# Performance work log

Measured on AMD Instinct MI355X. Metric: run time of the kernel, lower is better.

Reference implementation:

```python
import jax, jax.numpy as jnp
import numpy as np

N_U, N_P, E, E_LAB = 100000, 50000, 2000000, 500000
D_U, D_P, H = 64, 128, 64


def _seg_mean(feat, idx, n):
    # scatter-mean: sum per destination / clamp(count, 1)
    s = jax.ops.segment_sum(feat, idx, num_segments=n)
    c = jax.ops.segment_sum(jnp.ones((idx.shape[0],), feat.dtype), idx, num_segments=n)
    return s / jnp.maximum(c, 1.0)[:, None]


def setup_inputs() -> dict:
    key = jax.random.key(0)
    ks = jax.random.split(key, 16)
    inp = {
        'x_user': jax.random.normal(ks[0], (N_U, D_U), jnp.float32),
        'x_product': jax.random.normal(ks[1], (N_P, D_P), jnp.float32),
        'W1_buys_l': jax.random.normal(ks[2], (D_U, H), jnp.float32) * 0.05,
        'b1_buys': jnp.zeros((H,), jnp.float32),
        'W1_buys_r': jax.random.normal(ks[3], (D_P, H), jnp.float32) * 0.05,
        'W1_rev_l': jax.random.normal(ks[4], (D_P, H), jnp.float32) * 0.05,
        'b1_rev': jnp.zeros((H,), jnp.float32),
        'W1_rev_r': jax.random.normal(ks[5], (D_U, H), jnp.float32) * 0.05,
        'W2_buys_l': jax.random.normal(ks[6], (H, H), jnp.float32) * 0.05,
        'b2_buys': jnp.zeros((H,), jnp.float32),
        'W2_buys_r': jax.random.normal(ks[7], (H, H), jnp.float32) * 0.05,
        'W2_rev_l': jax.random.normal(ks[8], (H, H), jnp.float32) * 0.05,
        'b2_rev': jnp.zeros((H,), jnp.float32),
        'W2_rev_r': jax.random.normal(ks[9], (H, H), jnp.float32) * 0.05,
        'edge_src': jax.random.randint(ks[10], (E,), 0, N_U, jnp.int32),
        'edge_dst': jax.random.randint(ks[11], (E,), 0, N_P, jnp.int32),
        'lab_u': jax.random.randint(ks[12], (E_LAB,), 0, N_U, jnp.int32),
        'lab_p': jax.random.randint(ks[13], (E_LAB,), 0, N_P, jnp.int32),
    }
    return inp


def reference(x_user, x_product, W1_buys_l, b1_buys, W1_buys_r, W1_rev_l, b1_rev, W1_rev_r,
              W2_buys_l, b2_buys, W2_buys_r, W2_rev_l, b2_rev, W2_rev_r,
              edge_src, edge_dst, lab_u, lab_p):
    # SAGEConv (mean aggr): out_dst = mean_agg(x_src) @ W_l + b + x_dst @ W_r
    def sage(x_src, x_dst, src, dst, n_dst, Wl, b, Wr):
        agg = _seg_mean(x_src[src], dst, n_dst)
        return agg @ Wl + b + x_dst @ Wr

    n_u, n_p = x_user.shape[0], x_product.shape[0]
    # layer 1 (per edge type, hetero) + relu
    h_p = jax.nn.relu(sage(x_user, x_product, edge_src, edge_dst, n_p, W1_buys_l, b1_buys, W1_buys_r))
    h_u = jax.nn.relu(sage(x_product, x_user, edge_dst, edge_src, n_u, W1_rev_l, b1_rev, W1_rev_r))
    # layer 2
    h_p2 = sage(h_u, h_p, edge_src, edge_dst, n_p, W2_buys_l, b2_buys, W2_buys_r)
    h_u2 = sage(h_p, h_u, edge_dst, edge_src, n_u, W2_rev_l, b2_rev, W2_rev_r)
    # classifier: per-label-edge dot product
    return jnp.sum(h_u2[lab_u] * h_p2[lab_p], axis=-1)
```

## Files before the change

### kernel.cpp

```cpp
#include <hip/hip_runtime.h>


using u16 = unsigned short;
using u32 = unsigned int;

__device__ __forceinline__ u16 bf16r(float f) {
    u32 b = __float_as_uint(f);
    b += 0x7fffu + ((b >> 16) & 1u);
    return (u16)(b >> 16);
}
__device__ __forceinline__ float bflo(u32 u) { return __uint_as_float(u << 16); }
__device__ __forceinline__ float bfhi(u32 u) { return __uint_as_float(u & 0xffff0000u); }

#define BSH 8
#define MAXB 512
#define CHUNK 4096
#define RPT 16

__global__ __launch_bounds__(256) void k_partCast(
    const int* __restrict__ keysP, const int* __restrict__ payP,
    int* __restrict__ curPp, uint2* __restrict__ pairsP, int NBP, int SLP,
    const int* __restrict__ keysU, const int* __restrict__ payU,
    int* __restrict__ curUp, uint2* __restrict__ pairsU, int NBU, int SLU,
    int E, int pblocks,
    const int* __restrict__ keysL,
    int* __restrict__ curLp, uint2* __restrict__ pairsL, int NBL, int SLL,
    int EL, int lblocks,
    const float* __restrict__ xc, u16* __restrict__ yc, int n8) {
    __shared__ int hist[MAXB];
    __shared__ int sA[MAXB];
    __shared__ int sB[MAXB];
    __shared__ int bx[MAXB];
    __shared__ int gbase[MAXB];
    __shared__ uint2 prs[CHUNK];
    int tid = threadIdx.x;
    int bix = blockIdx.x;
    if (bix >= 2 * pblocks + lblocks) {
        int i = (bix - 2 * pblocks - lblocks) * 256 + tid;
        if (i < n8) {
            const float4* x4 = (const float4*)xc;
            float4 a = x4[i * 2], b = x4[i * 2 + 1];
            uint4 o;
            o.x = (u32)bf16r(a.x) | ((u32)bf16r(a.y) << 16);
            o.y = (u32)bf16r(a.z) | ((u32)bf16r(a.w) << 16);
            o.z = (u32)bf16r(b.x) | ((u32)bf16r(b.y) << 16);
            o.w = (u32)bf16r(b.z) | ((u32)bf16r(b.w) << 16);
            ((uint4*)yc)[i] = o;
        }
        return;
    }
    const int* keys; const int* pay; int* cursor; uint2* pairs;
    int NB, SL, cb, nE;
    if (bix < pblocks) {
        keys = keysP; pay = payP; cursor = curPp; pairs = pairsP; NB = NBP; SL = SLP;
        cb = bix; nE = E;
    } else if (bix < 2 * pblocks) {
        keys = keysU; pay = payU; cursor = curUp; pairs = pairsU; NB = NBU; SL = SLU;
        cb = bix - pblocks; nE = E;
    } else {
        keys = keysL; pay = nullptr; cursor = curLp; pairs = pairsL; NB = NBL; SL = SLL;
        cb = bix - 2 * pblocks; nE = EL;
    }
    int i0 = cb * CHUNK;
    int count = min(CHUNK, nE - i0);
    for (int i = tid; i < MAXB; i += 256) hist[i] = 0;
    __syncthreads();
    int keyr[RPT], payr[RPT], rankr[RPT];
#pragma unroll
    for (int r = 0; r < RPT; ++r) {
        int idx = r * 256 + tid;
        if (idx < count) {
            int k = keys[i0 + idx];
            keyr[r] = k;
            payr[r] = pay ? pay[i0 + idx] : (i0 + idx);
            rankr[r] = atomicAdd(&hist[k >> BSH], 1);
        } else keyr[r] = -1;
    }
    __syncthreads();
    sA[tid] = hist[tid]; sA[tid + 256] = hist[tid + 256];
    __syncthreads();
    int* src = sA; int* dst = sB;
    for (int off = 1; off < MAXB; off <<= 1) {
        dst[tid] = src[tid] + ((tid >= off) ? src[tid - off] : 0);
        int i2 = tid + 256;
        dst[i2] = src[i2] + ((i2 >= off) ? src[i2 - off] : 0);
        __syncthreads();
        int* t = src; src = dst; dst = t;
    }
    bx[tid] = src[tid] - hist[tid];
    bx[tid + 256] = src[tid + 256] - hist[tid + 256];
    __syncthreads();
    for (int b = tid; b < NB; b += 256) {
        int c = hist[b];
        gbase[b] = c ? (b * SL + atomicAdd(&cursor[b], c)) : 0;
    }
#pragma unroll
    for (int r = 0; r < RPT; ++r) {
        if (keyr[r] >= 0)
            prs[bx[keyr[r] >> BSH] + rankr[r]] = make_uint2((u32)keyr[r], (u32)payr[r]);
    }
    __syncthreads();
    for (int j = tid; j < count; j += 256) {
        uint2 pr = prs[j];
        int b = pr.x >> BSH;
        pairs[gbase[b] + (j - bx[b])] = pr;
    }
}

__global__ __launch_bounds__(256) void k_bucketFill(
    const uint2* __restrict__ pairsP, const int* __restrict__ cntP, int NBP, int SLP,
    int* __restrict__ nbr_p, int* __restrict__ deg_p, int* __restrict__ ptr_p, int NP,
    const uint2* __restrict__ pairsU, const int* __restrict__ cntU, int NBU, int SLU,
    int* __restrict__ nbr_u, int* __restrict__ deg_u, int* __restrict__ ptr_u, int NU) {
    const uint2* pairs; const int* cntA; int* nbr; int* deg; int* ptr;
    int N, SL, bucket;
    if ((int)blockIdx.x < NBP) {
        pairs = pairsP; cntA = cntP; nbr = nbr_p; deg = deg_p; ptr = ptr_p; N = NP;
        SL = SLP; bucket = blockIdx.x;
    } else {
        pairs = pairsU; cntA = cntU; nbr = nbr_u; deg = deg_u; ptr = ptr_u; N = NU;
        SL = SLU; bucket = blockIdx.x - NBP;
    }
    int tid = threadIdx.x;
    int base = bucket * SL;
    int cnt = cntA[bucket];
    __shared__ int h[256];
    __shared__ int s[256];
    __shared__ int cur[256];
    h[tid] = 0;
    __syncthreads();
    for (int j = tid; j < cnt; j += 256) atomicAdd(&h[pairs[base + j].x & 255], 1);
    __syncthreads();
    int d = h[tid];
    s[tid] = d;
    __syncthreads();
    for (int off = 1; off < 256; off <<= 1) {
        int v = (tid >= off) ? s[tid - off] : 0;
        __syncthreads();
        s[tid] += v;
        __syncthreads();
    }
    int excl = s[tid] - d;
    int node = bucket * 256 + tid;
    if (node < N) { deg[node] = d; ptr[node] = base + excl; }
    cur[tid] = excl;
    __syncthreads();
    for (int j = tid; j < cnt; j += 256) {
        uint2 pr = pairs[base + j];
        int pos = atomicAdd(&cur[pr.x & 255], 1);
        nbr[base + pos] = (int)(pr.y << 7);
    }
}

#define ACC8(A0,A1,A2,A3,A4,A5,A6,A7,V) \
    A0 += bflo((V).x); A1 += bfhi((V).x); A2 += bflo((V).y); A3 += bfhi((V).y); \
    A4 += bflo((V).z); A5 += bfhi((V).z); A6 += bflo((V).w); A7 += bfhi((V).w);

__global__ __launch_bounds__(256) void k_gather2(
    const u16* __restrict__ yA, const int* __restrict__ nbrA, const int* __restrict__ stpA,
    const int* __restrict__ degA, float* __restrict__ aggA, int NA,
    const u16* __restrict__ yB, const int* __restrict__ nbrB, const int* __restrict__ stpB,
    const int* __restrict__ degB, float* __restrict__ aggB, int NB) {
    int w = (blockIdx.x * 256 + threadIdx.x) >> 6;
    int lane = threadIdx.x & 63;
    if (w >= NA + NB) return;
    const u16* y; const int* nbr; const int* stp; const int* deg; float* agg; int n;
    if (w < NA) { y = yA; nbr = nbrA; stp = stpA; deg = degA; agg = aggA; n = w; }
    else        { y = yB; nbr = nbrB; stp = stpB; deg = degB; agg = aggB; n = w - NA; }
    const int q = lane >> 3, t = lane & 7;
    const int d = deg[n];
    const int st = stp[n];
    const char* yb = (const char*)y + t * 16;
    float a0=0,a1=0,a2=0,a3=0,a4=0,a5=0,a6=0,a7=0;
    for (int j = 0; j < d; j += 64) {
        const int cnt = min(d - j, 64);
        int offv = 0;
        if (lane < cnt) offv = nbr[st + j + lane];
#define GLD(R) \
        int g##R = __shfl(offv, R * 8 + q, 64); \
        uint4 v##R = make_uint4(0u, 0u, 0u, 0u); \
        if (R * 8 + q < cnt) v##R = *(const uint4*)(yb + g##R);
        GLD(0) GLD(1) GLD(2) GLD(3) GLD(4) GLD(5) GLD(6) GLD(7)
#undef GLD
#define ACCR(R) if (R * 8 < cnt) { ACC8(a0,a1,a2,a3,a4,a5,a6,a7,v##R) }
        ACCR(0) ACCR(1) ACCR(2) ACCR(3) ACCR(4) ACCR(5) ACCR(6) ACCR(7)
#undef ACCR
    }
#pragma unroll
    for (int m = 8; m < 64; m <<= 1) {
        a0 += __shfl_xor(a0, m, 64); a1 += __shfl_xor(a1, m, 64);
        a2 += __shfl_xor(a2, m, 64); a3 += __shfl_xor(a3, m, 64);
        a4 += __shfl_xor(a4, m, 64); a5 += __shfl_xor(a5, m, 64);
        a6 += __shfl_xor(a6, m, 64); a7 += __shfl_xor(a7, m, 64);
    }
    if (q == 0) {
        float dinv = 1.0f / (float)max(d, 1);
        float* dstp = agg + n * 64 + t * 8;
        *(float4*)dstp       = make_float4(a0 * dinv, a1 * dinv, a2 * dinv, a3 * dinv);
        *(float4*)(dstp + 4) = make_float4(a4 * dinv, a5 * dinv, a6 * dinv, a7 * dinv);
    }
}

#define FMA_ROW(ACC, O, W4) \
    ACC[0] += (O) * (W4).x; ACC[1] += (O) * (W4).y; \
    ACC[2] += (O) * (W4).z; ACC[3] += (O) * (W4).w;

template <int K, bool PRE, bool BIAS, bool RELU, bool EMIT>
__global__ __launch_bounds__(256) void k_ctilePairX(
    const float* __restrict__ pre0, const float* __restrict__ bias0,
    const float* __restrict__ x0, const float* __restrict__ W0,
    float* __restrict__ h0, u16* __restrict__ hbf0, int N0, int g0,
    const float* __restrict__ pre1, const float* __restrict__ bias1,
    const float* __restrict__ x1, const float* __restrict__ W1,
    float* __restrict__ h1, u16* __restrict__ hbf1, int N1) {
    constexpr int ROWS = (K == 64) ? 64 : 32;
    constexpr int RR = ROWS / 16;
    constexpr int STRIDE = K + 4;
    constexpr int KF4 = K / 4;
    __shared__ float Ws[K * 64];
    __shared__ float op[ROWS * STRIDE];
    const float* pre; const float* bias; const float* x; const float* W;
    float* h; u16* hbf;
    int N, bid, gsz;
    if ((int)blockIdx.x < g0) {
        pre = pre0; bias = bias0; x = x0; W = W0; h = h0; hbf = hbf0; N = N0;
        bid = blockIdx.x; gsz = g0;
    } else {
        pre = pre1; bias = bias1; x = x1; W = W1; h = h1; hbf = hbf1; N = N1;
        bid = blockIdx.x - g0; gsz = gridDim.x - g0;
    }
    const int tid = threadIdx.x;
    for (int i = tid; i < K * 16; i += 256)
        ((float4*)Ws)[i] = ((const float4*)W)[i];
    const int c4 = (tid & 15) * 4;
    const int rb = (tid >> 4) * RR;
    float bx_ = 0.f, by_ = 0.f, bz_ = 0.f, bw_ = 0.f;
    if (BIAS) {
        float4 b4 = *(const float4*)(bias + c4);
        bx_ = b4.x; by_ = b4.y; bz_ = b4.z; bw_ = b4.w;
    }
    const int ntiles = (N + ROWS - 1) / ROWS;
    for (int tile = bid; tile < ntiles; tile += gsz) {
        const int row0 = tile * ROWS;
        __syncthreads();
        for (int i = tid; i < ROWS * KF4; i += 256) {
            int r = i / KF4, k4 = (i % KF4) * 4;
            int row = row0 + r;
            float4 v = make_float4(0.f, 0.f, 0.f, 0.f);
            if (row < N) v = *(const float4*)(x + (size_t)row * K + k4);
            *(float4*)(op + r * STRIDE + k4) = v;
        }
        __syncthreads();
        float acc[RR][4];
#pragma unroll
        for (int i = 0; i < RR; ++i) {
            float px = 0.f, py = 0.f, pz = 0.f, pw = 0.f;
            if (PRE) {
                int row = row0 + rb + i;
                if (row < N) {
                    float4 p = *(const float4*)(pre + row * 64 + c4);
                    px = p.x; py = p.y; pz = p.z; pw = p.w;
                }
            }
            acc[i][0] = bx_ + px; acc[i][1] = by_ + py;
            acc[i][2] = bz_ + pz; acc[i][3] = bw_ + pw;
        }
        for (int kk = 0; kk < K; kk += 4) {
            float4 w0 = *(const float4*)(Ws + (kk + 0) * 64 + c4);
            float4 w1 = *(const float4*)(Ws + (kk + 1) * 64 + c4);
            float4 w2 = *(const float4*)(Ws + (kk + 2) * 64 + c4);
            float4 w3 = *(const float4*)(Ws + (kk + 3) * 64 + c4);
#pragma unroll
            for (int i = 0; i < RR; ++i) {
                float4 o = *(const float4*)(op + (rb + i) * STRIDE + kk);
                FMA_ROW(acc[i], o.x, w0);
                FMA_ROW(acc[i], o.y, w1);
                FMA_ROW(acc[i], o.z, w2);
                FMA_ROW(acc[i], o.w, w3);
            }
        }
#pragma unroll
        for (int i = 0; i < RR; ++i) {
            int row = row0 + rb + i;
            if (row >= N) continue;
            float v0 = acc[i][0], v1 = acc[i][1], v2 = acc[i][2], v3 = acc[i][3];
            if (RELU) {
                v0 = fmaxf(v0, 0.f); v1 = fmaxf(v1, 0.f);
                v2 = fmaxf(v2, 0.f); v3 = fmaxf(v3, 0.f);
            }
            *(float4*)(h + row * 64 + c4) = make_float4(v0, v1, v2, v3);
            if (EMIT) {
                uint2 o;
                o.x = (u32)bf16r(v0) | ((u32)bf16r(v1) << 16);
                o.y = (u32)bf16r(v2) | ((u32)bf16r(v3) << 16);
                *(uint2*)(hbf + row * 64 + c4) = o;
            }
        }
    }
}

template <bool BIAS>
__global__ __launch_bounds__(256) void k_ctilePairCat(
    const float* __restrict__ bias0, const float* __restrict__ xa0,
    const float* __restrict__ xb0, const float* __restrict__ Wa0,
    const float* __restrict__ Wb0, float* __restrict__ h0, int N0, int g0,
    const float* __restrict__ bias1, const float* __restrict__ xa1,
    const float* __restrict__ xb1, const float* __restrict__ Wa1,
    const float* __restrict__ Wb1, float* __restrict__ h1, int N1) {
    constexpr int ROWS = 32, RR = 2, STRIDE = 132, KF4 = 32;
    __shared__ float Ws[128 * 64];
    __shared__ float op[ROWS * STRIDE];
    const float* bias; const float* xa; const float* xb;
    const float* Wa; const float* Wb; float* h;
    int N, bid, gsz;
    if ((int)blockIdx.x < g0) {
        bias = bias0; xa = xa0; xb = xb0; Wa = Wa0; Wb = Wb0; h = h0; N = N0;
        bid = blockIdx.x; gsz = g0;
    } else {
        bias = bias1; xa = xa1; xb = xb1; Wa = Wa1; Wb = Wb1; h = h1; N = N1;
        bid = blockIdx.x - g0; gsz = gridDim.x - g0;
    }
    const int tid = threadIdx.x;
    for (int i = tid; i < 64 * 16; i += 256) {
        ((float4*)Ws)[i]           = ((const float4*)Wa)[i];
        ((float4*)Ws)[64 * 16 + i] = ((const float4*)Wb)[i];
    }
    const int c4 = (tid & 15) * 4;
    const int rb = (tid >> 4) * RR;
    float bx_ = 0.f, by_ = 0.f, bz_ = 0.f, bw_ = 0.f;
    if (BIAS) {
        float4 b4 = *(const float4*)(bias + c4);
        bx_ = b4.x; by_ = b4.y; bz_ = b4.z; bw_ = b4.w;
    }
    const int ntiles = (N + ROWS - 1) / ROWS;
    for (int tile = bid; tile < ntiles; tile += gsz) {
        const int row0 = tile * ROWS;
        __syncthreads();
        for (int i = tid; i < ROWS * KF4; i += 256) {
            int r = i >> 5, k4 = (i & 31) * 4;
            int row = row0 + r;
            float4 v = make_float4(0.f, 0.f, 0.f, 0.f);
            if (row < N)
                v = (k4 < 64) ? *(const float4*)(xa + (size_t)row * 64 + k4)
                              : *(const float4*)(xb + (size_t)row * 64 + (k4 - 64));
            *(float4*)(op + r * STRIDE + k4) = v;
        }
        __syncthreads();
        float acc[RR][4];
#pragma unroll
        for (int i = 0; i < RR; ++i) {
            acc[i][0] = bx_; acc[i][1] = by_; acc[i][2] = bz_; acc[i][3] = bw_;
        }
        for (int kk = 0; kk < 128; kk += 4) {
            float4 w0 = *(const float4*)(Ws + (kk + 0) * 64 + c4);
            float4 w1 = *(const float4*)(Ws + (kk + 1) * 64 + c4);
            float4 w2 = *(const float4*)(Ws + (kk + 2) * 64 + c4);
            float4 w3 = *(const float4*)(Ws + (kk + 3) * 64 + c4);
#pragma unroll
            for (int i = 0; i < RR; ++i) {
                float4 o = *(const float4*)(op + (rb + i) * STRIDE + kk);
                FMA_ROW(acc[i], o.x, w0);
                FMA_ROW(acc[i], o.y, w1);
                FMA_ROW(acc[i], o.z, w2);
                FMA_ROW(acc[i], o.w, w3);
            }
        }
#pragma unroll
        for (int i = 0; i < RR; ++i) {
            int row = row0 + rb + i;
            if (row >= N) continue;
            *(float4*)(h + row * 64 + c4) =
                make_float4(acc[i][0], acc[i][1], acc[i][2], acc[i][3]);
        }
    }
}

__global__ __launch_bounds__(256) void k_classifyS(const float* __restrict__ hu,
                                                   const float* __restrict__ hp,
                                                   const int* __restrict__ lu,
                                                   const uint2* __restrict__ pairsL,
                                                   const int* __restrict__ cntL,
                                                   int lsh,
                                                   float* __restrict__ out, int nslots) {
    int w = (blockIdx.x * 256 + threadIdx.x) >> 6;
    int lane = threadIdx.x & 63;
    int q = lane >> 4, t = lane & 15;
    int slot = w * 4 + q;
    float v = 0.f;
    int e = 0;
    bool ok = false;
    if (slot < nslots) {
        int bucket = slot >> lsh;
        int within = slot & ((1 << lsh) - 1);
        if (within < cntL[bucket]) {
            uint2 pr = pairsL[slot];
            int p = (int)pr.x;
            e = (int)pr.y;
            int u = lu[e];
            float4 a = *(const float4*)(hu + (size_t)u * 64 + t * 4);
            float4 b = *(const float4*)(hp + (size_t)p * 64 + t * 4);
            v = a.x * b.x + a.y * b.y + a.z * b.z + a.w * b.w;
            ok = true;
        }
    }
#pragma unroll
    for (int m = 1; m < 16; m <<= 1) v += __shfl_xor(v, m, 64);
    if (t == 0 && ok) out[e] = v;
}

extern "C" void kernel_launch(void* const* d_in, const int* in_sizes, int n_in,
                              void* d_out, int out_size, void* d_ws, size_t ws_size,
                              hipStream_t stream) {
    const float* x_user    = (const float*)d_in[0];
    const float* x_product = (const float*)d_in[1];
    const float* W1bl = (const float*)d_in[2];
    const float* b1b  = (const float*)d_in[3];
    const float* W1br = (const float*)d_in[4];
    const float* W1rl = (const float*)d_in[5];
    const float* b1r  = (const float*)d_in[6];
    const float* W1rr = (const float*)d_in[7];
    const float* W2bl = (const float*)d_in[8];
    const float* b2b  = (const float*)d_in[9];
    const float* W2br = (const float*)d_in[10];
    const float* W2rl = (const float*)d_in[11];
    const float* b2r  = (const float*)d_in[12];
    const float* W2rr = (const float*)d_in[13];
    const int* esrc = (const int*)d_in[14];
    const int* edst = (const int*)d_in[15];
    const int* lu   = (const int*)d_in[16];
    const int* lp   = (const int*)d_in[17];

    const int NU = in_sizes[0] / 64;
    const int NP = in_sizes[1] / 128;
    const int E  = in_sizes[14];
    const int EL = in_sizes[16];
    const int NBP = (NP + 255) >> BSH;
    const int NBU = (NU + 255) >> BSH;
    const int NBL = NBP;

    const int SLP = E / NBP + E / (NBP * 8) + 1024;
    const int SLU = E / NBU + E / (NBU * 8) + 1024;
    int lneed = EL / NBL + EL / (NBL * 4) + 512;
    int lsh = 1;
    while ((1 << lsh) < lneed) ++lsh;
    const int SLL = 1 << lsh;

    char* ws = (char*)d_ws;
    size_t off = 0;
    auto alloc = [&](size_t bytes) -> void* {
        void* p = ws + off;
        off += (bytes + 255) & ~(size_t)255;
        return p;
    };
    int*   deg_u  = (int*)alloc((size_t)NU * 4);
    int*   deg_p  = (int*)alloc((size_t)NP * 4);
    int*   ptr_u  = (int*)alloc((size_t)NU * 4);
    int*   ptr_p  = (int*)alloc((size_t)NP * 4);
    int*   curP   = (int*)alloc((size_t)MAXB * 4);
    int*   curU   = (int*)alloc((size_t)MAXB * 4);
    int*   curL   = (int*)alloc((size_t)MAXB * 4);
    int*   nbr_u  = (int*)alloc((size_t)NBU * SLU * 4);
    int*   nbr_p  = (int*)alloc((size_t)NBP * SLP * 4);
    uint2* pairsL = (uint2*)alloc((size_t)NBL * SLL * 8);
    size_t aggBytes = (size_t)(NP + NU) * 64 * 4;
    size_t pairBytes = ((size_t)NBP * SLP + (size_t)NBU * SLU) * 8;
    char* uni = (char*)alloc(aggBytes > pairBytes ? aggBytes : pairBytes);
    float* aggP   = (float*)uni;
    float* aggU   = (float*)(uni + (size_t)NP * 64 * 4);
    uint2* pairsP = (uint2*)uni;
    uint2* pairsU = (uint2*)(uni + (size_t)NBP * SLP * 8);
    u16*   bfA    = (u16*)alloc((size_t)NU * 64 * 2);
    u16*   bfB    = (u16*)alloc((size_t)NP * 64 * 2);
    float* h_p    = (float*)alloc((size_t)NP * 64 * 4);
    float* h_u    = (float*)alloc((size_t)NU * 64 * 4);
    float* sinkF  = h_u;
    u16*   sinkB  = (u16*)((char*)h_u + (size_t)NP * 64 * 4);

    hipMemsetAsync(curP, 0, (size_t)MAXB * 3 * 4, stream);
    const int n8 = NU * 64 / 8;
    const int castBlocks = (n8 + 255) / 256;
    const int pblocks = (E + CHUNK - 1) / CHUNK;
    const int lblocks = (EL + CHUNK - 1) / CHUNK;
    k_partCast<<<2 * pblocks + lblocks + castBlocks, 256, 0, stream>>>(
        edst, esrc, curP, pairsP, NBP, SLP,
        esrc, edst, curU, pairsU, NBU, SLU, E, pblocks,
        lp, curL, pairsL, NBL, SLL, EL, lblocks,
        x_user, bfA, n8);
    k_bucketFill<<<NBP + NBU, 256, 0, stream>>>(
        pairsP, curP, NBP, SLP, nbr_p, deg_p, ptr_p, NP,
        pairsU, curU, NBU, SLU, nbr_u, deg_u, ptr_u, NU);

    const int tP32 = (NP + 31) / 32;
    const int tU32 = (NU + 31) / 32;
    const int tP64 = (NP + 63) / 64, tU64 = (NU + 63) / 64;
    auto cap = [](int t, int c) { return t < c ? t : c; };

    {
        const int g0 = cap(tP32, 768);
        k_ctilePairX<128, false, false, false, true><<<g0 + cap(tP32, 768), 256, 0, stream>>>(
            nullptr, nullptr, x_product, W1rl, sinkF, bfB, NP, g0,
            nullptr, nullptr, x_product, W1br, h_p, sinkB, NP);
    }

    k_gather2<<<(NP + NU + 3) / 4, 256, 0, stream>>>(bfA, nbr_p, ptr_p, deg_p, aggP, NP,
                                                     bfB, nbr_u, ptr_u, deg_u, aggU, NU);
    {
        const int gP = cap(tP64, 512), gU = cap(tU64, 1024);
        k_ctilePairX<64, true, true, true, true><<<gP + gU, 256, 0, stream>>>(
            h_p, b1b, aggP, W1bl, h_p, bfB, NP, gP,
            aggU, b1r, x_user, W1rr, h_u, bfA, NU);
    }

    k_gather2<<<(NP + NU + 3) / 4, 256, 0, stream>>>(bfA, nbr_p, ptr_p, deg_p, aggP, NP,
                                                     bfB, nbr_u, ptr_u, deg_u, aggU, NU);
    {
        const int gP = cap(tP32, 512), gU = cap(tU32, 1024);
        k_ctilePairCat<true><<<gP + gU, 256, 0, stream>>>(
            b2b, aggP, h_p, W2bl, W2br, h_p, NP, gP,
            b2r, aggU, h_u, W2rl, W2rr, h_u, NU);
    }

    const int nslots = NBL << lsh;
    k_classifyS<<<((nslots + 3) / 4 + 3) / 4, 256, 0, stream>>>(
        h_u, h_p, lu, pairsL, curL, lsh, (float*)d_out, nslots);
}
```

Before: 482.0 us.

## Fold first product projection GEMM into partition/cast kernel launch

The separate K=128 projection kernel for x_product (W1_rev_l to bf16 and W1_buys_r to h_p) becomes extra blocks appended to the partition/cast launch, with shared memory unioned into one 49 KB buffer. This removes a kernel launch and lets the GEMM blocks overlap with the partitioning work. It also raises the static shared memory of every partition block, which may lower occupancy for the sorting path. The gather accumulators are regrouped into float2 pairs, likely to encourage packed adds.

```diff
diff --git a/kernel.cpp b/kernel.cpp
--- a/kernel.cpp
+++ b/kernel.cpp
@@ -9,13 +9,18 @@
     b += 0x7fffu + ((b >> 16) & 1u);
     return (u16)(b >> 16);
 }
-__device__ __forceinline__ float bflo(u32 u) { return __uint_as_float(u << 16); }
-__device__ __forceinline__ float bfhi(u32 u) { return __uint_as_float(u & 0xffff0000u); }
+__device__ __forceinline__ float2 bfup(u32 u) {
+    return make_float2(__uint_as_float(u << 16), __uint_as_float(u & 0xffff0000u));
+}
 
 #define BSH 8
 #define MAXB 512
 #define CHUNK 4096
 #define RPT 16
+
+#define FMA_ROW(ACC, O, W4) \
+    ACC[0] += (O) * (W4).x; ACC[1] += (O) * (W4).y; \
+    ACC[2] += (O) * (W4).z; ACC[3] += (O) * (W4).w;
 
 __global__ __launch_bounds__(256) void k_partCast(
     const int* __restrict__ keysP, const int* __restrict__ payP,
@@ -26,15 +31,72 @@
     const int* __restrict__ keysL,
     int* __restrict__ curLp, uint2* __restrict__ pairsL, int NBL, int SLL,
     int EL, int lblocks,
-    const float* __restrict__ xc, u16* __restrict__ yc, int n8) {
-    __shared__ int hist[MAXB];
-    __shared__ int sA[MAXB];
-    __shared__ int sB[MAXB];
-    __shared__ int bx[MAXB];
-    __shared__ int gbase[MAXB];
-    __shared__ uint2 prs[CHUNK];
+    const float* __restrict__ xc, u16* __restrict__ yc, int n8,
+    int ctStart, int g128,
+    const float* __restrict__ xp, const float* __restrict__ Wrl,
+    const float* __restrict__ Wbr, u16* __restrict__ bfB,
+    float* __restrict__ h_p, float* __restrict__ sinkF,
+    u16* __restrict__ sinkB, int NPc) {
+    __shared__ __align__(16) char smem[49664];
     int tid = threadIdx.x;
     int bix = blockIdx.x;
+    if (bix >= ctStart) {
+        float* Ws = (float*)smem;
+        float* op = (float*)(smem + 32768);
+        int cbix = bix - ctStart;
+        const float* W; float* h; u16* hbf;
+        int bid;
+        if (cbix < g128) { W = Wrl; h = sinkF; hbf = bfB;   bid = cbix; }
+        else             { W = Wbr; h = h_p;   hbf = sinkB; bid = cbix - g128; }
+        for (int i = tid; i < 128 * 16; i += 256)
+            ((float4*)Ws)[i] = ((const float4*)W)[i];
+        const int c4 = (tid & 15) * 4;
+        const int rb = (tid >> 4) * 2;
+        const int ntiles = (NPc + 31) / 32;
+        for (int tile = bid; tile < ntiles; tile += g128) {
+            const int row0 = tile * 32;
+            __syncthreads();
+            for (int i = tid; i < 32 * 32; i += 256) {
+                int r = i >> 5, k4 = (i & 31) * 4;
+                int row = row0 + r;
+                float4 v = make_float4(0.f, 0.f, 0.f, 0.f);
+                if (row < NPc) v = *(const float4*)(xp + (size_t)row * 128 + k4);
+                *(float4*)(op + r * 132 + k4) = v;
+            }
+            __syncthreads();
+            float acc[2][4];
+#pragma unroll
+            for (int i = 0; i < 2; ++i) {
+                acc[i][0] = 0.f; acc[i][1] = 0.f; acc[i][2] = 0.f; acc[i][3] = 0.f;
+            }
+            for (int kk = 0; kk < 128; kk += 4) {
+                float4 w0 = *(const float4*)(Ws + (kk + 0) * 64 + c4);
+                float4 w1 = *(const float4*)(Ws + (kk + 1) * 64 + c4);
+                float4 w2 = *(const float4*)(Ws + (kk + 2) * 64 + c4);
+                float4 w3 = *(const float4*)(Ws + (kk + 3) * 64 + c4);
+#pragma unroll
+                for (int i = 0; i < 2; ++i) {
+                    float4 o = *(const float4*)(op + (rb + i) * 132 + kk);
+                    FMA_ROW(acc[i], o.x, w0);
+                    FMA_ROW(acc[i], o.y, w1);
+                    FMA_ROW(acc[i], o.z, w2);
+                    FMA_ROW(acc[i], o.w, w3);
+                }
+            }
+#pragma unroll
+            for (int i = 0; i < 2; ++i) {
+                int row = row0 + rb + i;
+                if (row >= NPc) continue;
+                float v0 = acc[i][0], v1 = acc[i][1], v2 = acc[i][2], v3 = acc[i][3];
+                *(float4*)(h + (size_t)row * 64 + c4) = make_float4(v0, v1, v2, v3);
+                uint2 o;
+                o.x = (u32)bf16r(v0) | ((u32)bf16r(v1) << 16);
+                o.y = (u32)bf16r(v2) | ((u32)bf16r(v3) << 16);
+                *(uint2*)(hbf + (size_t)row * 64 + c4) = o;
+            }
+        }
+        return;
+    }
     if (bix >= 2 * pblocks + lblocks) {
         int i = (bix - 2 * pblocks - lblocks) * 256 + tid;
         if (i < n8) {
@@ -49,6 +111,12 @@
         }
         return;
     }
+    int* hist   = (int*)smem;
+    int* sA     = (int*)(smem + 2048);
+    int* sB     = (int*)(smem + 4096);
+    int* bx     = (int*)(smem + 6144);
+    int* gbase  = (int*)(smem + 8192);
+    uint2* prs  = (uint2*)(smem + 10240);
     const int* keys; const int* pay; int* cursor; uint2* pairs;
     int NB, SL, cb, nE;
     if (bix < pblocks) {
@@ -152,9 +220,8 @@
     }
 }
 
-#define ACC8(A0,A1,A2,A3,A4,A5,A6,A7,V) \
-    A0 += bflo((V).x); A1 += bfhi((V).x); A2 += bflo((V).y); A3 += bfhi((V).y); \
-    A4 += bflo((V).z); A5 += bfhi((V).z); A6 += bflo((V).w); A7 += bfhi((V).w);
+#define ACC8(A01,A23,A45,A67,V) \
+    A01 += bfup((V).x); A23 += bfup((V).y); A45 += bfup((V).z); A67 += bfup((V).w);
 
 __global__ __launch_bounds__(256) void k_gather2(
     const u16* __restrict__ yA, const int* __restrict__ nbrA, const int* __restrict__ stpA,
@@ -171,7 +238,8 @@
     const int d = deg[n];
     const int st = stp[n];
     const char* yb = (const char*)y + t * 16;
-    float a0=0,a1=0,a2=0,a3=0,a4=0,a5=0,a6=0,a7=0;
+    float2 a01 = make_float2(0.f, 0.f), a23 = make_float2(0.f, 0.f);
+    float2 a45 = make_float2(0.f, 0.f), a67 = make_float2(0.f, 0.f);
     for (int j = 0; j < d; j += 64) {
         const int cnt = min(d - j, 64);
         int offv = 0;
@@ -182,28 +250,24 @@
         if (R * 8 + q < cnt) v##R = *(const uint4*)(yb + g##R);
         GLD(0) GLD(1) GLD(2) GLD(3) GLD(4) GLD(5) GLD(6) GLD(7)
 #undef GLD
-#define ACCR(R) if (R * 8 < cnt) { ACC8(a0,a1,a2,a3,a4,a5,a6,a7,v##R) }
+#define ACCR(R) if (R * 8 < cnt) { ACC8(a01,a23,a45,a67,v##R) }
         ACCR(0) ACCR(1) ACCR(2) ACCR(3) ACCR(4) ACCR(5) ACCR(6) ACCR(7)
 #undef ACCR
     }
 #pragma unroll
     for (int m = 8; m < 64; m <<= 1) {
-        a0 += __shfl_xor(a0, m, 64); a1 += __shfl_xor(a1, m, 64);
-        a2 += __shfl_xor(a2, m, 64); a3 += __shfl_xor(a3, m, 64);
-        a4 += __shfl_xor(a4, m, 64); a5 += __shfl_xor(a5, m, 64);
-        a6 += __shfl_xor(a6, m, 64); a7 += __shfl_xor(a7, m, 64);
+        a01.x += __shfl_xor(a01.x, m, 64); a01.y += __shfl_xor(a01.y, m, 64);
+        a23.x += __shfl_xor(a23.x, m, 64); a23.y += __shfl_xor(a23.y, m, 64);
+        a45.x += __shfl_xor(a45.x, m, 64); a45.y += __shfl_xor(a45.y, m, 64);
+        a67.x += __shfl_xor(a67.x, m, 64); a67.y += __shfl_xor(a67.y, m, 64);
     }
     if (q == 0) {
         float dinv = 1.0f / (float)max(d, 1);
         float* dstp = agg + n * 64 + t * 8;
-        *(float4*)dstp       = make_float4(a0 * dinv, a1 * dinv, a2 * dinv, a3 * dinv);
-        *(float4*)(dstp + 4) = make_float4(a4 * dinv, a5 * dinv, a6 * dinv, a7 * dinv);
-    }
-}
-
-#define FMA_ROW(ACC, O, W4) \
-    ACC[0] += (O) * (W4).x; ACC[1] += (O) * (W4).y; \
-    ACC[2] += (O) * (W4).z; ACC[3] += (O) * (W4).w;
+        *(float4*)dstp       = make_float4(a01.x * dinv, a01.y * dinv, a23.x * dinv, a23.y * dinv);
+        *(float4*)(dstp + 4) = make_float4(a45.x * dinv, a45.y * dinv, a67.x * dinv, a67.y * dinv);
+    }
+}
 
 template <int K, bool PRE, bool BIAS, bool RELU, bool EMIT>
 __global__ __launch_bounds__(256) void k_ctilePairX(
@@ -476,31 +540,28 @@
     float* sinkF  = h_u;
     u16*   sinkB  = (u16*)((char*)h_u + (size_t)NP * 64 * 4);
 
+    const int tP32 = (NP + 31) / 32;
+    const int tU32 = (NU + 31) / 32;
+    const int tP64 = (NP + 63) / 64, tU64 = (NU + 63) / 64;
+    auto cap = [](int t, int c) { return t < c ? t : c; };
+
     hipMemsetAsync(curP, 0, (size_t)MAXB * 3 * 4, stream);
     const int n8 = NU * 64 / 8;
     const int castBlocks = (n8 + 255) / 256;
     const int pblocks = (E + CHUNK - 1) / CHUNK;
     const int lblocks = (EL + CHUNK - 1) / CHUNK;
-    k_partCast<<<2 * pblocks + lblocks + castBlocks, 256, 0, stream>>>(
+    const int g128 = cap(tP32, 768);
+    const int ctStart = 2 * pblocks + lblocks + castBlocks;
+    k_partCast<<<ctStart + 2 * g128, 256, 0, stream>>>(
         edst, esrc, curP, pairsP, NBP, SLP,
         esrc, edst, curU, pairsU, NBU, SLU, E, pblocks,
         lp, curL, pairsL, NBL, SLL, EL, lblocks,
-        x_user, bfA, n8);
+        x_user, bfA, n8,
+        ctStart, g128,
+        x_product, W1rl, W1br, bfB, h_p, sinkF, sinkB, NP);
     k_bucketFill<<<NBP + NBU, 256, 0, stream>>>(
         pairsP, curP, NBP, SLP, nbr_p, deg_p, ptr_p, NP,
         pairsU, curU, NBU, SLU, nbr_u, deg_u, ptr_u, NU);
-
-    const int tP32 = (NP + 31) / 32;
-    const int tU32 = (NU + 31) / 32;
-    const int tP64 = (NP + 63) / 64, tU64 = (NU + 63) / 64;
-    auto cap = [](int t, int c) { return t < c ? t : c; };
-
-    {
-        const int g0 = cap(tP32, 768);
-        k_ctilePairX<128, false, false, false, true><<<g0 + cap(tP32, 768), 256, 0, stream>>>(
-            nullptr, nullptr, x_product, W1rl, sinkF, bfB, NP, g0,
-            nullptr, nullptr, x_product, W1br, h_p, sinkB, NP);
-    }
 
     k_gather2<<<(NP + NU + 3) / 4, 256, 0, stream>>>(bfA, nbr_p, ptr_p, deg_p, aggP, NP,
                                                      bfB, nbr_u, ptr_u, deg_u, aggU, NU);
```

After: 481.2 us. About the same (-0.2%).
